# Kernel tuning notes

Hardware: AMD Instinct MI355X
Metric: run time of the kernel (lower is better)

## Reference

```python
import jax, jax.numpy as jnp
import numpy as np

EPS = 1e-5
TAU = 2.0
HEADS = 8
SCALE = 0.125


def _bn(y, g, b, m, v):
    # y: [TB, C, N]; per-channel eval-mode batchnorm
    inv = jax.lax.rsqrt(v + EPS)
    return (y - m[:, None]) * (g * inv)[:, None] + b[:, None]


def _lif(x_seq, vth):
    # spikingjelly MultiStepLIFNode: v += (x - v)/tau, spike = H(v - vth), hard reset v*(1-s)
    def step(mem, xt):
        mem = mem + (xt - mem) / TAU
        s = (mem >= vth).astype(xt.dtype)
        mem = mem * (1.0 - s)
        return mem, s
    _, spikes = jax.lax.scan(step, jnp.zeros_like(x_seq[0]), x_seq)
    return spikes


def setup_inputs() -> dict:
    key = jax.random.key(0)
    ks = jax.random.split(key, 8)
    T, B, C, H, W = 4, 16, 256, 32, 32
    d = {
        'x': jax.random.normal(ks[0], (T, B, C, H, W), jnp.float32),
        'res_attn': jnp.zeros((1,), jnp.float32),
    }
    for i, p in enumerate(['q', 'k', 'v']):
        d[p + '_w'] = jax.random.normal(ks[1 + i], (C, C), jnp.float32) * 0.02
        d[p + '_gamma'] = jnp.ones((C,), jnp.float32)
        d[p + '_beta'] = jnp.zeros((C,), jnp.float32)
        d[p + '_mean'] = jnp.zeros((C,), jnp.float32)
        d[p + '_var'] = jnp.ones((C,), jnp.float32)
    d['p_w'] = jax.random.normal(ks[4], (C, C), jnp.float32) * 0.02
    d['p_b'] = jnp.zeros((C,), jnp.float32)
    d['p_gamma'] = jnp.ones((C,), jnp.float32)
    d['p_beta'] = jnp.zeros((C,), jnp.float32)
    d['p_mean'] = jnp.zeros((C,), jnp.float32)
    d['p_var'] = jnp.ones((C,), jnp.float32)
    return d


def reference(x, res_attn, q_w, q_gamma, q_beta, q_mean, q_var,
              k_w, k_gamma, k_beta, k_mean, k_var,
              v_w, v_gamma, v_beta, v_mean, v_var,
              p_w, p_b, p_gamma, p_beta, p_mean, p_var):
    T, B, C, H, W = x.shape
    N = H * W
    d = C // HEADS
    x2 = x.reshape(T * B, C, N)

    def branch(w, g, b, m, v):
        y = _bn(jnp.einsum('oc,bcn->bon', w, x2), g, b, m, v).reshape(T, B, C, N)
        s = _lif(y, 1.0)  # [T,B,C,N]
        # -> [T,B,heads,N,d]
        return s.transpose(0, 1, 3, 2).reshape(T, B, N, HEADS, d).transpose(0, 1, 3, 2, 4)

    q = branch(q_w, q_gamma, q_beta, q_mean, q_var)
    k = branch(k_w, k_gamma, k_beta, k_mean, k_var)
    v = branch(v_w, v_gamma, v_beta, v_mean, v_var)

    kv = jnp.einsum('tbhnd,tbhne->tbhde', k, v)      # [T,B,h,d,d]
    attn = jnp.einsum('tbhnd,tbhde->tbhne', q, kv) * SCALE  # [T,B,h,N,d]
    xa = attn.transpose(0, 1, 2, 4, 3).reshape(T, B, C, N)
    xa = _lif(xa, 0.5)

    y = _bn(jnp.einsum('oc,bcn->bon', p_w, xa.reshape(T * B, C, N)) + p_b[:, None],
            p_gamma, p_beta, p_mean, p_var)
    out = _lif(y.reshape(T, B, C, H, W), 1.0)
    return (out, v)
```

## Files before the change

kernel.cpp:

```cpp
#include <hip/hip_runtime.h>
#include <stdint.h>

typedef unsigned int u32;
typedef unsigned short ushort_t;

#define T_ 4
#define B_ 16
#define C_ 256
#define N_ 1024
#define CN (C_ * N_)
#define M_ELEMS (64 * C_ * N_)

#define OFF_S    0ull
#define OFF_XC   67108864ull
#define OFF_SC   67108864ull
#define OFF_KV   134217728ull
#define OFF_BNS  136314880ull
#define OFF_WC   136331264ull
#define OFF_WPC  137510912ull

typedef __attribute__((ext_vector_type(8))) short bf16x8;
typedef __attribute__((ext_vector_type(4))) float f32x4;

#define SWZ(c) (((c) & ~3) | (((c) & 3) ^ (((c) >> 2) & 3) ^ (((c) >> 4) & 3)))

__device__ __forceinline__ ushort_t f2bf(float f) {
  u32 u = __float_as_uint(f);
  u32 r = (u + 0x7FFFu + ((u >> 16) & 1u)) >> 16;
  return (ushort_t)r;
}
__device__ __forceinline__ float bf2f(ushort_t h) { return __uint_as_float((u32)h << 16); }

__device__ __forceinline__ void async_copy16(const void* g, void* l) {
  __builtin_amdgcn_global_load_lds(
      (const __attribute__((address_space(1))) u32*)g,
      (__attribute__((address_space(3))) u32*)l, 16, 0, 0);
}

__device__ __forceinline__ void mfma_grp(const ushort_t* Ap, int aoff,
                                         bf16x8 b0, bf16x8 b1, bf16x8 b2, bf16x8 b3,
                                         f32x4* acc) {
  bf16x8 a0 = *(const bf16x8*)&Ap[aoff + 0 * 16 * 32];
  bf16x8 a1 = *(const bf16x8*)&Ap[aoff + 1 * 16 * 32];
  bf16x8 a2 = *(const bf16x8*)&Ap[aoff + 2 * 16 * 32];
  bf16x8 a3 = *(const bf16x8*)&Ap[aoff + 3 * 16 * 32];
  acc[0]  = __builtin_amdgcn_mfma_f32_16x16x32_bf16(a0, b0, acc[0],  0, 0, 0);
  acc[1]  = __builtin_amdgcn_mfma_f32_16x16x32_bf16(a0, b1, acc[1],  0, 0, 0);
  acc[2]  = __builtin_amdgcn_mfma_f32_16x16x32_bf16(a0, b2, acc[2],  0, 0, 0);
  acc[3]  = __builtin_amdgcn_mfma_f32_16x16x32_bf16(a0, b3, acc[3],  0, 0, 0);
  acc[4]  = __builtin_amdgcn_mfma_f32_16x16x32_bf16(a1, b0, acc[4],  0, 0, 0);
  acc[5]  = __builtin_amdgcn_mfma_f32_16x16x32_bf16(a1, b1, acc[5],  0, 0, 0);
  acc[6]  = __builtin_amdgcn_mfma_f32_16x16x32_bf16(a1, b2, acc[6],  0, 0, 0);
  acc[7]  = __builtin_amdgcn_mfma_f32_16x16x32_bf16(a1, b3, acc[7],  0, 0, 0);
  acc[8]  = __builtin_amdgcn_mfma_f32_16x16x32_bf16(a2, b0, acc[8],  0, 0, 0);
  acc[9]  = __builtin_amdgcn_mfma_f32_16x16x32_bf16(a2, b1, acc[9],  0, 0, 0);
  acc[10] = __builtin_amdgcn_mfma_f32_16x16x32_bf16(a2, b2, acc[10], 0, 0, 0);
  acc[11] = __builtin_amdgcn_mfma_f32_16x16x32_bf16(a2, b3, acc[11], 0, 0, 0);
  acc[12] = __builtin_amdgcn_mfma_f32_16x16x32_bf16(a3, b0, acc[12], 0, 0, 0);
  acc[13] = __builtin_amdgcn_mfma_f32_16x16x32_bf16(a3, b1, acc[13], 0, 0, 0);
  acc[14] = __builtin_amdgcn_mfma_f32_16x16x32_bf16(a3, b2, acc[14], 0, 0, 0);
  acc[15] = __builtin_amdgcn_mfma_f32_16x16x32_bf16(a3, b3, acc[15], 0, 0, 0);
}

__global__ void bn_prep(const float* __restrict__ qg, const float* __restrict__ qb2, const float* __restrict__ qm, const float* __restrict__ qv,
                        const float* __restrict__ kg, const float* __restrict__ kb, const float* __restrict__ km, const float* __restrict__ kvv,
                        const float* __restrict__ vg, const float* __restrict__ vb, const float* __restrict__ vm, const float* __restrict__ vv,
                        const float* __restrict__ pbias,
                        const float* __restrict__ pg, const float* __restrict__ pbt, const float* __restrict__ pm, const float* __restrict__ pv,
                        float* __restrict__ bns) {
  int i = threadIdx.x;
  int br = i >> 8, c = i & 255;
  const float *g, *bt, *m, *v;
  float bias = 0.f;
  if (br == 0)      { g = qg; bt = qb2; m = qm; v = qv; }
  else if (br == 1) { g = kg; bt = kb;  m = km; v = kvv; }
  else if (br == 2) { g = vg; bt = vb;  m = vm; v = vv; }
  else              { g = pg; bt = pbt; m = pm; v = pv; bias = pbias[c]; }
  float sc = g[c] / sqrtf(v[c] + 1e-5f);
  float sh = bt[c] + (bias - m[c]) * sc;
  float rcp = (sc != 0.f) ? (1.f / sc) : 0.f;
  *(float4*)&bns[4 * i] = make_float4(sc, sh, rcp, 0.f);
}

__global__ __launch_bounds__(256) void convert_w(const float* __restrict__ qw, const float* __restrict__ kw,
                                                 const float* __restrict__ vw, const float* __restrict__ pw,
                                                 ushort_t* __restrict__ Wc, ushort_t* __restrict__ Wpc) {
  int id = blockIdx.x * 256 + threadIdx.x;
  int br = id >> 16, o = (id >> 8) & 255, c = id & 255;
  const float* w = (br == 0) ? qw : (br == 1) ? kw : (br == 2) ? vw : pw;
  float f = w[o * 256 + c];
  ushort_t hi = f2bf(f);
  ushort_t lo = f2bf(f - bf2f(hi));
  if (br < 3) {
    ushort_t* d = Wc + (size_t)br * 196608 + (size_t)o * 768 + c;
    d[0] = hi; d[256] = lo; d[512] = hi;
  } else {
    ushort_t* d = Wpc + (size_t)o * 512 + c;
    d[0] = hi; d[256] = lo;
  }
}

__global__ __launch_bounds__(256) void convert_x(const float* __restrict__ x, ushort_t* __restrict__ Xc) {
  __shared__ ushort_t hi[32][260];
  __shared__ ushort_t lo[32][260];
  int bid = blockIdx.x;
  int nc = bid & 3, kb = (bid >> 2) & 7, tb = bid >> 5;
  int t = threadIdx.x;
  int n0 = nc * 256;
  const float* xb = x + (size_t)tb * CN + (size_t)(kb * 32) * N_ + n0;
#pragma unroll
  for (int p = 0; p < 8; ++p) {
    int k = p * 4 + (t >> 6);
    int n4 = (t & 63) * 4;
    float4 v = *(const float4*)&xb[(size_t)k * N_ + n4];
    ushort_t h0 = f2bf(v.x), h1 = f2bf(v.y), h2 = f2bf(v.z), h3 = f2bf(v.w);
    short4 hv = make_short4((short)h0, (short)h1, (short)h2, (short)h3);
    short4 lv = make_short4((short)f2bf(v.x - bf2f(h0)), (short)f2bf(v.y - bf2f(h1)),
                            (short)f2bf(v.z - bf2f(h2)), (short)f2bf(v.w - bf2f(h3)));
    *(short4*)&hi[k][n4] = hv;
    *(short4*)&lo[k][n4] = lv;
  }
  __syncthreads();
  ushort_t* Hs = Xc + ((size_t)(tb * 16 + kb) * 1024 + n0) * 32;
  ushort_t* Ls = Xc + ((size_t)(tb * 16 + 8 + kb) * 1024 + n0) * 32;
  int kq = t & 3;
#pragma unroll
  for (int q = 0; q < 4; ++q) {
    int n = q * 64 + (t >> 2);
    u32 a0 = (u32)hi[kq * 8 + 0][n] | ((u32)hi[kq * 8 + 1][n] << 16);
    u32 a1 = (u32)hi[kq * 8 + 2][n] | ((u32)hi[kq * 8 + 3][n] << 16);
    u32 a2 = (u32)hi[kq * 8 + 4][n] | ((u32)hi[kq * 8 + 5][n] << 16);
    u32 a3 = (u32)hi[kq * 8 + 6][n] | ((u32)hi[kq * 8 + 7][n] << 16);
    *(uint4*)(Hs + (size_t)n * 32 + kq * 8) = make_uint4(a0, a1, a2, a3);
    u32 b0 = (u32)lo[kq * 8 + 0][n] | ((u32)lo[kq * 8 + 1][n] << 16);
    u32 b1 = (u32)lo[kq * 8 + 2][n] | ((u32)lo[kq * 8 + 3][n] << 16);
    u32 b2 = (u32)lo[kq * 8 + 4][n] | ((u32)lo[kq * 8 + 5][n] << 16);
    u32 b3 = (u32)lo[kq * 8 + 6][n] | ((u32)lo[kq * 8 + 7][n] << 16);
    *(uint4*)(Ls + (size_t)n * 32 + kq * 8) = make_uint4(b0, b1, b2, b3);
  }
}

__global__ __launch_bounds__(256, 3) void gemm_qkv_lif(
    const ushort_t* __restrict__ Wc, const ushort_t* __restrict__ Xc,
    const float* __restrict__ bns, uint8_t* __restrict__ S) {
  __shared__ ushort_t Ah[2][4096];
  __shared__ ushort_t Xl[2][4096];
  __shared__ ushort_t Bh[2][4096];
  const int nt = blockIdx.x, mt = blockIdx.y, b = blockIdx.z;
  const int br = mt >> 1, rh = mt & 1;
  const ushort_t* Ab = Wc + (size_t)br * 196608 + (size_t)(rh * 128) * 768;
  const int tid = threadIdx.x;
  const int lane = tid & 63;
  const int quad = lane >> 4, r = lane & 15;
  const int w = tid >> 6;
  const int moff = (w & 1) * 64, noff = (w >> 1) * 64;
  const int c0 = tid, c1 = tid + 256;
  const int s0 = SWZ(c0), s1 = SWZ(c1);
  const int qx = quad ^ (r & 3) ^ ((r >> 2) & 3);
  const int aoff = (moff + r) * 32 + qx * 8;
  const int boff = (noff + r) * 32 + qx * 8;

  f32x4 acc[16];
#pragma unroll
  for (int f = 0; f < 16; ++f) acc[f] = (f32x4){0.f, 0.f, 0.f, 0.f};

  for (int t = 0; t < 4; ++t) {
    const ushort_t* Xtb = Xc + (size_t)(t * 16 + b) * 16 * 32768 + (size_t)(nt * 128) * 32;
    for (int p = 0; p < 4; ++p) {
      const ushort_t* AcH = Ab + p * 64;
      const ushort_t* AcL = Ab + 256 + p * 64;
      const ushort_t* Bh0 = Xtb + (size_t)(2 * p) * 32768;
      const ushort_t* Bh1 = Bh0 + 32768;
      async_copy16(AcH + (size_t)(c0 >> 2) * 768 + (s0 & 3) * 8,      &Ah[0][c0 * 8]);
      async_copy16(AcH + (size_t)(c1 >> 2) * 768 + (s1 & 3) * 8,      &Ah[0][c1 * 8]);
      async_copy16(AcH + (size_t)(c0 >> 2) * 768 + 32 + (s0 & 3) * 8, &Ah[1][c0 * 8]);
      async_copy16(AcH + (size_t)(c1 >> 2) * 768 + 32 + (s1 & 3) * 8, &Ah[1][c1 * 8]);
      async_copy16(AcL + (size_t)(c0 >> 2) * 768 + (s0 & 3) * 8,      &Xl[0][c0 * 8]);
      async_copy16(AcL + (size_t)(c1 >> 2) * 768 + (s1 & 3) * 8,      &Xl[0][c1 * 8]);
      async_copy16(AcL + (size_t)(c0 >> 2) * 768 + 32 + (s0 & 3) * 8, &Xl[1][c0 * 8]);
      async_copy16(AcL + (size_t)(c1 >> 2) * 768 + 32 + (s1 & 3) * 8, &Xl[1][c1 * 8]);
      async_copy16(Bh0 + s0 * 8, &Bh[0][c0 * 8]);
      async_copy16(Bh0 + s1 * 8, &Bh[0][c1 * 8]);
      async_copy16(Bh1 + s0 * 8, &Bh[1][c0 * 8]);
      async_copy16(Bh1 + s1 * 8, &Bh[1][c1 * 8]);
      __syncthreads();
      {
        bf16x8 b0 = *(const bf16x8*)&Bh[0][boff + 0 * 16 * 32];
        bf16x8 b1 = *(const bf16x8*)&Bh[0][boff + 1 * 16 * 32];
        bf16x8 b2 = *(const bf16x8*)&Bh[0][boff + 2 * 16 * 32];
        bf16x8 b3 = *(const bf16x8*)&Bh[0][boff + 3 * 16 * 32];
        mfma_grp(&Ah[0][0], aoff, b0, b1, b2, b3, acc);
        mfma_grp(&Xl[0][0], aoff, b0, b1, b2, b3, acc);
      }
      {
        bf16x8 b0 = *(const bf16x8*)&Bh[1][boff + 0 * 16 * 32];
        bf16x8 b1 = *(const bf16x8*)&Bh[1][boff + 1 * 16 * 32];
        bf16x8 b2 = *(const bf16x8*)&Bh[1][boff + 2 * 16 * 32];
        bf16x8 b3 = *(const bf16x8*)&Bh[1][boff + 3 * 16 * 32];
        mfma_grp(&Ah[1][0], aoff, b0, b1, b2, b3, acc);
        mfma_grp(&Xl[1][0], aoff, b0, b1, b2, b3, acc);
      }
      __syncthreads();
      const ushort_t* Bl0 = Xtb + (size_t)(8 + 2 * p) * 32768;
      const ushort_t* Bl1 = Bl0 + 32768;
      async_copy16(Bl0 + s0 * 8, &Xl[0][c0 * 8]);
      async_copy16(Bl0 + s1 * 8, &Xl[0][c1 * 8]);
      async_copy16(Bl1 + s0 * 8, &Xl[1][c0 * 8]);
      async_copy16(Bl1 + s1 * 8, &Xl[1][c1 * 8]);
      __syncthreads();
      {
        bf16x8 b0 = *(const bf16x8*)&Xl[0][boff + 0 * 16 * 32];
        bf16x8 b1 = *(const bf16x8*)&Xl[0][boff + 1 * 16 * 32];
        bf16x8 b2 = *(const bf16x8*)&Xl[0][boff + 2 * 16 * 32];
        bf16x8 b3 = *(const bf16x8*)&Xl[0][boff + 3 * 16 * 32];
        mfma_grp(&Ah[0][0], aoff, b0, b1, b2, b3, acc);
      }
      {
        bf16x8 b0 = *(const bf16x8*)&Xl[1][boff + 0 * 16 * 32];
        bf16x8 b1 = *(const bf16x8*)&Xl[1][boff + 1 * 16 * 32];
        bf16x8 b2 = *(const bf16x8*)&Xl[1][boff + 2 * 16 * 32];
        bf16x8 b3 = *(const bf16x8*)&Xl[1][boff + 3 * 16 * 32];
        mfma_grp(&Ah[1][0], aoff, b0, b1, b2, b3, acc);
      }
      __syncthreads();
    }
    uint8_t* Sb = S + (size_t)br * M_ELEMS + (size_t)(t * 16 + b) * CN;
#pragma unroll
    for (int i = 0; i < 4; ++i) {
#pragma unroll
      for (int rg = 0; rg < 4; ++rg) {
        int c = rh * 128 + moff + i * 16 + quad * 4 + rg;
        float4 bn = *(const float4*)&bns[4 * (br * 256 + c)];
        float hsc = 0.5f * bn.x;
        float hsh = 0.5f * bn.y;
        float rcp = bn.z;
        uint8_t* row = Sb + (size_t)c * N_ + nt * 128 + noff + r;
#pragma unroll
        for (int j = 0; j < 4; ++j) {
          float m = acc[i * 4 + j][rg] * hsc + hsh;
          uint8_t s = (m >= 1.0f) ? 1 : 0;
          row[j * 16] = s;
          acc[i * 4 + j][rg] = s ? 0.f : m * rcp;
        }
      }
    }
  }
}

__global__ __launch_bounds__(256) void transpose_v(const uint8_t* __restrict__ SV, float* __restrict__ vout) {
  size_t o4 = ((size_t)blockIdx.x * 256 + threadIdx.x) * 4;
  int dd = (int)(o4 & 31);
  int n = (int)((o4 >> 5) & 1023);
  int h = (int)((o4 >> 15) & 7);
  int tb = (int)(o4 >> 18);
  const uint8_t* src = SV + (size_t)tb * CN + (size_t)(h * 32 + dd) * N_ + n;
  *(float4*)(vout + o4) = make_float4((float)src[0], (float)src[(size_t)N_],
                                      (float)src[2 * (size_t)N_], (float)src[3 * (size_t)N_]);
}

__global__ __launch_bounds__(256) void kv_gram(const uint8_t* __restrict__ SK,
                                               const uint8_t* __restrict__ SV,
                                               float* __restrict__ KV) {
  __shared__ unsigned long long Kb[32][17];
  __shared__ unsigned long long Vb[32][17];
  const int tb = blockIdx.x >> 3, h = blockIdx.x & 7;
  const uint8_t* K = SK + (size_t)tb * CN + (size_t)h * 32 * N_;
  const uint8_t* V = SV + (size_t)tb * CN + (size_t)h * 32 * N_;
  const int tid = threadIdx.x;
  const int row = tid >> 3, c8 = tid & 7;
  uint8_t* Kb8 = (uint8_t*)&Kb[row][0];
  uint8_t* Vb8 = (uint8_t*)&Vb[row][0];
#pragma unroll
  for (int i = 0; i < 16; ++i) {
    int c = c8 + 8 * i;
    unsigned long long xk = *(const unsigned long long*)(K + (size_t)row * N_ + (size_t)c * 8);
    unsigned long long xv = *(const unsigned long long*)(V + (size_t)row * N_ + (size_t)c * 8);
    Kb8[c] = (uint8_t)((xk * 0x8040201008040201ull) >> 56);
    Vb8[c] = (uint8_t)((xv * 0x8040201008040201ull) >> 56);
  }
  __syncthreads();
  const int dd = tid >> 3, e0 = (tid & 7) * 4;
  int a0 = 0, a1 = 0, a2 = 0, a3 = 0;
#pragma unroll
  for (int c = 0; c < 16; ++c) {
    unsigned long long kd = Kb[dd][c];
    a0 += __popcll(kd & Vb[e0 + 0][c]);
    a1 += __popcll(kd & Vb[e0 + 1][c]);
    a2 += __popcll(kd & Vb[e0 + 2][c]);
    a3 += __popcll(kd & Vb[e0 + 3][c]);
  }
  float* o = KV + (size_t)(tb * 8 + h) * 1024 + dd * 32 + e0;
  o[0] = (float)a0; o[1] = (float)a1; o[2] = (float)a2; o[3] = (float)a3;
}

__global__ __launch_bounds__(256) void attn_lif(const uint8_t* __restrict__ SQ,
                                                const float* __restrict__ KV,
                                                ushort_t* __restrict__ Sc) {
  __shared__ float kvs[1024];
  const int bid = blockIdx.x;
  const int nb = bid & 15, h = (bid >> 4) & 7, b = bid >> 7;
  const int n0 = nb * 64;
  const int tid = threadIdx.x;
  const int nl = tid & 63, eg = tid >> 6;
  float mem[8];
#pragma unroll
  for (int j = 0; j < 8; ++j) mem[j] = 0.f;
  for (int t = 0; t < 4; ++t) {
    const float* kvp = KV + (size_t)((t * B_ + b) * 8 + h) * 1024;
    *(float4*)&kvs[tid * 4] = *(const float4*)&kvp[tid * 4];
    __syncthreads();
    const uint8_t* q = SQ + (size_t)(t * B_ + b) * CN + (size_t)h * 32 * N_ + n0 + nl;
    float val[8];
#pragma unroll
    for (int j = 0; j < 8; ++j) val[j] = 0.f;
#pragma unroll 4
    for (int dd = 0; dd < 32; ++dd) {
      float qv = (float)q[(size_t)dd * N_];
#pragma unroll
      for (int j = 0; j < 8; ++j) val[j] += qv * kvs[dd * 32 + eg * 8 + j];
    }
    ushort_t pk[8];
#pragma unroll
    for (int j = 0; j < 8; ++j) {
      float a = val[j] * 0.125f;
      mem[j] += (a - mem[j]) * 0.5f;
      int s = (mem[j] >= 0.5f);
      pk[j] = s ? (ushort_t)0x3F80 : (ushort_t)0;
      if (s) mem[j] = 0.f;
    }
    uint4 o;
    o.x = (u32)pk[0] | ((u32)pk[1] << 16);
    o.y = (u32)pk[2] | ((u32)pk[3] << 16);
    o.z = (u32)pk[4] | ((u32)pk[5] << 16);
    o.w = (u32)pk[6] | ((u32)pk[7] << 16);
    *(uint4*)(Sc + ((size_t)((t * B_ + b) * 8 + h) * 1024 + n0 + nl) * 32 + eg * 8) = o;
    __syncthreads();
  }
}

__global__ __launch_bounds__(256, 3) void gemm_p_lif(
    const ushort_t* __restrict__ Wpc, const ushort_t* __restrict__ Sc,
    const float* __restrict__ bns, float* __restrict__ out) {
  __shared__ ushort_t Ah[2][4096];
  __shared__ ushort_t Al[2][4096];
  __shared__ ushort_t Bs[2][4096];
  const int nt = blockIdx.x, mt = blockIdx.y, b = blockIdx.z;
  const ushort_t* Ab = Wpc + (size_t)(mt * 128) * 512;
  const int tid = threadIdx.x;
  const int lane = tid & 63;
  const int quad = lane >> 4, r = lane & 15;
  const int w = tid >> 6;
  const int moff = (w & 1) * 64, noff = (w >> 1) * 64;
  const int c0 = tid, c1 = tid + 256;
  const int s0 = SWZ(c0), s1 = SWZ(c1);
  const int qx = quad ^ (r & 3) ^ ((r >> 2) & 3);
  const int aoff = (moff + r) * 32 + qx * 8;
  const int boff = (noff + r) * 32 + qx * 8;
  f32x4 acc[16];
#pragma unroll
  for (int f = 0; f < 16; ++f) acc[f] = (f32x4){0.f, 0.f, 0.f, 0.f};

  for (int t = 0; t < 4; ++t) {
    const ushort_t* Stb = Sc + (size_t)(t * 16 + b) * 8 * 32768 + (size_t)(nt * 128) * 32;
    for (int p = 0; p < 4; ++p) {
      const ushort_t* AcH = Ab + p * 64;
      const ushort_t* AcL = Ab + 256 + p * 64;
      const ushort_t* Bb0 = Stb + (size_t)(2 * p) * 32768;
      const ushort_t* Bb1 = Bb0 + 32768;
      async_copy16(AcH + (size_t)(c0 >> 2) * 512 + (s0 & 3) * 8,      &Ah[0][c0 * 8]);
      async_copy16(AcH + (size_t)(c1 >> 2) * 512 + (s1 & 3) * 8,      &Ah[0][c1 * 8]);
      async_copy16(AcH + (size_t)(c0 >> 2) * 512 + 32 + (s0 & 3) * 8, &Ah[1][c0 * 8]);
      async_copy16(AcH + (size_t)(c1 >> 2) * 512 + 32 + (s1 & 3) * 8, &Ah[1][c1 * 8]);
      async_copy16(AcL + (size_t)(c0 >> 2) * 512 + (s0 & 3) * 8,      &Al[0][c0 * 8]);
      async_copy16(AcL + (size_t)(c1 >> 2) * 512 + (s1 & 3) * 8,      &Al[0][c1 * 8]);
      async_copy16(AcL + (size_t)(c0 >> 2) * 512 + 32 + (s0 & 3) * 8, &Al[1][c0 * 8]);
      async_copy16(AcL + (size_t)(c1 >> 2) * 512 + 32 + (s1 & 3) * 8, &Al[1][c1 * 8]);
      async_copy16(Bb0 + s0 * 8, &Bs[0][c0 * 8]);
      async_copy16(Bb0 + s1 * 8, &Bs[0][c1 * 8]);
      async_copy16(Bb1 + s0 * 8, &Bs[1][c0 * 8]);
      async_copy16(Bb1 + s1 * 8, &Bs[1][c1 * 8]);
      __syncthreads();
      {
        bf16x8 b0 = *(const bf16x8*)&Bs[0][boff + 0 * 16 * 32];
        bf16x8 b1 = *(const bf16x8*)&Bs[0][boff + 1 * 16 * 32];
        bf16x8 b2 = *(const bf16x8*)&Bs[0][boff + 2 * 16 * 32];
        bf16x8 b3 = *(const bf16x8*)&Bs[0][boff + 3 * 16 * 32];
        mfma_grp(&Ah[0][0], aoff, b0, b1, b2, b3, acc);
        mfma_grp(&Al[0][0], aoff, b0, b1, b2, b3, acc);
      }
      {
        bf16x8 b0 = *(const bf16x8*)&Bs[1][boff + 0 * 16 * 32];
        bf16x8 b1 = *(const bf16x8*)&Bs[1][boff + 1 * 16 * 32];
        bf16x8 b2 = *(const bf16x8*)&Bs[1][boff + 2 * 16 * 32];
        bf16x8 b3 = *(const bf16x8*)&Bs[1][boff + 3 * 16 * 32];
        mfma_grp(&Ah[1][0], aoff, b0, b1, b2, b3, acc);
        mfma_grp(&Al[1][0], aoff, b0, b1, b2, b3, acc);
      }
      __syncthreads();
    }
    float* Ob = out + (size_t)(t * 16 + b) * CN;
#pragma unroll
    for (int i = 0; i < 4; ++i) {
#pragma unroll
      for (int rg = 0; rg < 4; ++rg) {
        int c = mt * 128 + moff + i * 16 + quad * 4 + rg;
        float4 bn = *(const float4*)&bns[4 * (768 + c)];
        float hsc = 0.5f * bn.x;
        float hsh = 0.5f * bn.y;
        float rcp = bn.z;
        float* row2 = Ob + (size_t)c * N_ + nt * 128 + noff + r;
#pragma unroll
        for (int j = 0; j < 4; ++j) {
          float m = acc[i * 4 + j][rg] * hsc + hsh;
          int s = (m >= 1.0f);
          row2[j * 16] = s ? 1.0f : 0.0f;
          acc[i * 4 + j][rg] = s ? 0.f : m * rcp;
        }
      }
    }
  }
}

extern "C" void kernel_launch(void* const* d_in, const int* in_sizes, int n_in,
                              void* d_out, int out_size, void* d_ws, size_t ws_size,
                              hipStream_t stream) {
  const float* x   = (const float*)d_in[0];
  const float* qw  = (const float*)d_in[2];
  const float* qg  = (const float*)d_in[3];
  const float* qb  = (const float*)d_in[4];
  const float* qm  = (const float*)d_in[5];
  const float* qv  = (const float*)d_in[6];
  const float* kw  = (const float*)d_in[7];
  const float* kg  = (const float*)d_in[8];
  const float* kb  = (const float*)d_in[9];
  const float* km  = (const float*)d_in[10];
  const float* kvv = (const float*)d_in[11];
  const float* vw  = (const float*)d_in[12];
  const float* vg  = (const float*)d_in[13];
  const float* vb  = (const float*)d_in[14];
  const float* vm  = (const float*)d_in[15];
  const float* vv  = (const float*)d_in[16];
  const float* pw  = (const float*)d_in[17];
  const float* pb  = (const float*)d_in[18];
  const float* pg  = (const float*)d_in[19];
  const float* pbt = (const float*)d_in[20];
  const float* pm  = (const float*)d_in[21];
  const float* pv  = (const float*)d_in[22];

  float* out = (float*)d_out;
  float* vout = out + M_ELEMS;

  uint8_t* ws = (uint8_t*)d_ws;
  uint8_t* S   = ws + OFF_S;
  ushort_t* Xc = (ushort_t*)(ws + OFF_XC);
  ushort_t* Sc = (ushort_t*)(ws + OFF_SC);
  float* KV    = (float*)(ws + OFF_KV);
  float* BNS   = (float*)(ws + OFF_BNS);
  ushort_t* Wc  = (ushort_t*)(ws + OFF_WC);
  ushort_t* Wpc = (ushort_t*)(ws + OFF_WPC);

  bn_prep<<<dim3(1), dim3(1024), 0, stream>>>(qg, qb, qm, qv, kg, kb, km, kvv,
                                              vg, vb, vm, vv, pb, pg, pbt, pm, pv, BNS);
  convert_w<<<dim3(1024), dim3(256), 0, stream>>>(qw, kw, vw, pw, Wc, Wpc);
  convert_x<<<dim3(2048), dim3(256), 0, stream>>>(x, Xc);
  gemm_qkv_lif<<<dim3(8, 6, 16), dim3(256), 0, stream>>>(Wc, Xc, BNS, S);
  transpose_v<<<dim3(16384), dim3(256), 0, stream>>>(S + 2ull * M_ELEMS, vout);
  kv_gram<<<dim3(512), dim3(256), 0, stream>>>(S + 1ull * M_ELEMS, S + 2ull * M_ELEMS, KV);
  attn_lif<<<dim3(2048), dim3(256), 0, stream>>>(S, KV, Sc);
  gemm_p_lif<<<dim3(8, 2, 16), dim3(256), 0, stream>>>(Wpc, Sc, BNS, out);
}
```

Baseline: 404.9 us.

## Pipeline QKV and projection GEMM K-loops with a three-buffer async prefetch ring

Both LIF-fused GEMM kernels replace their load-everything-then-compute inner loops with a flat loop over K=32 stages. Each stage loads an A chunk and a B chunk into one of three LDS buffers, prefetching two stages ahead. Explicit vmcnt waits and raw s_barrier calls replace the per-phase __syncthreads, so global-to-LDS copies overlap the MFMA work. This trades coarser load batches and manual wait-count bookkeeping for less stall time. The bookkeeping is fragile if other memory ops, such as the epilogue stores, shift the outstanding counts.

```diff
diff --git a/kernel.cpp b/kernel.cpp
--- a/kernel.cpp
+++ b/kernel.cpp
@@ -23,6 +23,8 @@
 typedef __attribute__((ext_vector_type(4))) float f32x4;
 
 #define SWZ(c) (((c) & ~3) | (((c) & 3) ^ (((c) >> 2) & 3) ^ (((c) >> 4) & 3)))
+
+#define WAITV(N) asm volatile("s_waitcnt vmcnt(" #N ")" ::: "memory")
 
 __device__ __forceinline__ ushort_t f2bf(float f) {
   u32 u = __float_as_uint(f);
@@ -143,9 +145,7 @@
 __global__ __launch_bounds__(256, 3) void gemm_qkv_lif(
     const ushort_t* __restrict__ Wc, const ushort_t* __restrict__ Xc,
     const float* __restrict__ bns, uint8_t* __restrict__ S) {
-  __shared__ ushort_t Ah[2][4096];
-  __shared__ ushort_t Xl[2][4096];
-  __shared__ ushort_t Bh[2][4096];
+  __shared__ ushort_t L[3][8192];
   const int nt = blockIdx.x, mt = blockIdx.y, b = blockIdx.z;
   const int br = mt >> 1, rh = mt & 1;
   const ushort_t* Ab = Wc + (size_t)br * 196608 + (size_t)(rh * 128) * 768;
@@ -158,89 +158,70 @@
   const int s0 = SWZ(c0), s1 = SWZ(c1);
   const int qx = quad ^ (r & 3) ^ ((r >> 2) & 3);
   const int aoff = (moff + r) * 32 + qx * 8;
-  const int boff = (noff + r) * 32 + qx * 8;
+  const int boff = 4096 + (noff + r) * 32 + qx * 8;
+
+  auto STAGE = [&](int gS, int bi) {
+    const int tS = gS / 24;
+    const int jS = gS - tS * 24;
+    const ushort_t* Acol = Ab + jS * 32;
+    const int slab = (jS < 8) ? jS : (jS - 8);
+    const ushort_t* Bb = Xc + ((size_t)(tS * 16 + b) * 16 + slab) * 32768 +
+                         (size_t)(nt * 128) * 32;
+    ushort_t* Lb = &L[bi][0];
+    async_copy16(Acol + (size_t)(c0 >> 2) * 768 + (s0 & 3) * 8, Lb + c0 * 8);
+    async_copy16(Acol + (size_t)(c1 >> 2) * 768 + (s1 & 3) * 8, Lb + c1 * 8);
+    async_copy16(Bb + s0 * 8, Lb + 4096 + c0 * 8);
+    async_copy16(Bb + s1 * 8, Lb + 4096 + c1 * 8);
+  };
 
   f32x4 acc[16];
 #pragma unroll
   for (int f = 0; f < 16; ++f) acc[f] = (f32x4){0.f, 0.f, 0.f, 0.f};
 
-  for (int t = 0; t < 4; ++t) {
-    const ushort_t* Xtb = Xc + (size_t)(t * 16 + b) * 16 * 32768 + (size_t)(nt * 128) * 32;
-    for (int p = 0; p < 4; ++p) {
-      const ushort_t* AcH = Ab + p * 64;
-      const ushort_t* AcL = Ab + 256 + p * 64;
-      const ushort_t* Bh0 = Xtb + (size_t)(2 * p) * 32768;
-      const ushort_t* Bh1 = Bh0 + 32768;
-      async_copy16(AcH + (size_t)(c0 >> 2) * 768 + (s0 & 3) * 8,      &Ah[0][c0 * 8]);
-      async_copy16(AcH + (size_t)(c1 >> 2) * 768 + (s1 & 3) * 8,      &Ah[0][c1 * 8]);
-      async_copy16(AcH + (size_t)(c0 >> 2) * 768 + 32 + (s0 & 3) * 8, &Ah[1][c0 * 8]);
-      async_copy16(AcH + (size_t)(c1 >> 2) * 768 + 32 + (s1 & 3) * 8, &Ah[1][c1 * 8]);
-      async_copy16(AcL + (size_t)(c0 >> 2) * 768 + (s0 & 3) * 8,      &Xl[0][c0 * 8]);
-      async_copy16(AcL + (size_t)(c1 >> 2) * 768 + (s1 & 3) * 8,      &Xl[0][c1 * 8]);
-      async_copy16(AcL + (size_t)(c0 >> 2) * 768 + 32 + (s0 & 3) * 8, &Xl[1][c0 * 8]);
-      async_copy16(AcL + (size_t)(c1 >> 2) * 768 + 32 + (s1 & 3) * 8, &Xl[1][c1 * 8]);
-      async_copy16(Bh0 + s0 * 8, &Bh[0][c0 * 8]);
-      async_copy16(Bh0 + s1 * 8, &Bh[0][c1 * 8]);
-      async_copy16(Bh1 + s0 * 8, &Bh[1][c0 * 8]);
-      async_copy16(Bh1 + s1 * 8, &Bh[1][c1 * 8]);
-      __syncthreads();
-      {
-        bf16x8 b0 = *(const bf16x8*)&Bh[0][boff + 0 * 16 * 32];
-        bf16x8 b1 = *(const bf16x8*)&Bh[0][boff + 1 * 16 * 32];
-        bf16x8 b2 = *(const bf16x8*)&Bh[0][boff + 2 * 16 * 32];
-        bf16x8 b3 = *(const bf16x8*)&Bh[0][boff + 3 * 16 * 32];
-        mfma_grp(&Ah[0][0], aoff, b0, b1, b2, b3, acc);
-        mfma_grp(&Xl[0][0], aoff, b0, b1, b2, b3, acc);
-      }
-      {
-        bf16x8 b0 = *(const bf16x8*)&Bh[1][boff + 0 * 16 * 32];
-        bf16x8 b1 = *(const bf16x8*)&Bh[1][boff + 1 * 16 * 32];
-        bf16x8 b2 = *(const bf16x8*)&Bh[1][boff + 2 * 16 * 32];
-        bf16x8 b3 = *(const bf16x8*)&Bh[1][boff + 3 * 16 * 32];
-        mfma_grp(&Ah[1][0], aoff, b0, b1, b2, b3, acc);
-        mfma_grp(&Xl[1][0], aoff, b0, b1, b2, b3, acc);
-      }
-      __syncthreads();
-      const ushort_t* Bl0 = Xtb + (size_t)(8 + 2 * p) * 32768;
-      const ushort_t* Bl1 = Bl0 + 32768;
-      async_copy16(Bl0 + s0 * 8, &Xl[0][c0 * 8]);
-      async_copy16(Bl0 + s1 * 8, &Xl[0][c1 * 8]);
-      async_copy16(Bl1 + s0 * 8, &Xl[1][c0 * 8]);
-      async_copy16(Bl1 + s1 * 8, &Xl[1][c1 * 8]);
-      __syncthreads();
-      {
-        bf16x8 b0 = *(const bf16x8*)&Xl[0][boff + 0 * 16 * 32];
-        bf16x8 b1 = *(const bf16x8*)&Xl[0][boff + 1 * 16 * 32];
-        bf16x8 b2 = *(const bf16x8*)&Xl[0][boff + 2 * 16 * 32];
-        bf16x8 b3 = *(const bf16x8*)&Xl[0][boff + 3 * 16 * 32];
-        mfma_grp(&Ah[0][0], aoff, b0, b1, b2, b3, acc);
-      }
-      {
-        bf16x8 b0 = *(const bf16x8*)&Xl[1][boff + 0 * 16 * 32];
-        bf16x8 b1 = *(const bf16x8*)&Xl[1][boff + 1 * 16 * 32];
-        bf16x8 b2 = *(const bf16x8*)&Xl[1][boff + 2 * 16 * 32];
-        bf16x8 b3 = *(const bf16x8*)&Xl[1][boff + 3 * 16 * 32];
-        mfma_grp(&Ah[1][0], aoff, b0, b1, b2, b3, acc);
-      }
-      __syncthreads();
-    }
-    uint8_t* Sb = S + (size_t)br * M_ELEMS + (size_t)(t * 16 + b) * CN;
-#pragma unroll
-    for (int i = 0; i < 4; ++i) {
-#pragma unroll
-      for (int rg = 0; rg < 4; ++rg) {
-        int c = rh * 128 + moff + i * 16 + quad * 4 + rg;
-        float4 bn = *(const float4*)&bns[4 * (br * 256 + c)];
-        float hsc = 0.5f * bn.x;
-        float hsh = 0.5f * bn.y;
-        float rcp = bn.z;
-        uint8_t* row = Sb + (size_t)c * N_ + nt * 128 + noff + r;
-#pragma unroll
-        for (int j = 0; j < 4; ++j) {
-          float m = acc[i * 4 + j][rg] * hsc + hsh;
-          uint8_t s = (m >= 1.0f) ? 1 : 0;
-          row[j * 16] = s;
-          acc[i * 4 + j][rg] = s ? 0.f : m * rcp;
+  STAGE(0, 0);
+  STAGE(1, 1);
+  int cb = 0, sb = 2;
+
+#pragma unroll 1
+  for (int g = 0; g < 96; ++g) {
+    __builtin_amdgcn_s_barrier();
+    __builtin_amdgcn_sched_barrier(0);
+    if (g < 94) STAGE(g + 2, sb);
+    if (g < 94)      { WAITV(8); }
+    else if (g == 94){ WAITV(4); }
+    else             { WAITV(0); }
+    __builtin_amdgcn_s_barrier();
+    __builtin_amdgcn_sched_barrier(0);
+    {
+      const ushort_t* Lc = &L[cb][0];
+      bf16x8 q0 = *(const bf16x8*)&Lc[boff + 0 * 512];
+      bf16x8 q1 = *(const bf16x8*)&Lc[boff + 1 * 512];
+      bf16x8 q2 = *(const bf16x8*)&Lc[boff + 2 * 512];
+      bf16x8 q3 = *(const bf16x8*)&Lc[boff + 3 * 512];
+      mfma_grp(Lc, aoff, q0, q1, q2, q3, acc);
+    }
+    cb = (cb == 2) ? 0 : cb + 1;
+    sb = (sb == 2) ? 0 : sb + 1;
+    const int t = g / 24;
+    if (g - t * 24 == 23) {
+      uint8_t* Sb = S + (size_t)br * M_ELEMS + (size_t)(t * 16 + b) * CN;
+#pragma unroll
+      for (int i = 0; i < 4; ++i) {
+#pragma unroll
+        for (int rg = 0; rg < 4; ++rg) {
+          int c = rh * 128 + moff + i * 16 + quad * 4 + rg;
+          float4 bn = *(const float4*)&bns[4 * (br * 256 + c)];
+          float hsc = 0.5f * bn.x;
+          float hsh = 0.5f * bn.y;
+          float rcp = bn.z;
+          uint8_t* row = Sb + (size_t)c * N_ + nt * 128 + noff + r;
+#pragma unroll
+          for (int j = 0; j < 4; ++j) {
+            float m = acc[i * 4 + j][rg] * hsc + hsh;
+            uint8_t s = (m >= 1.0f) ? 1 : 0;
+            row[j * 16] = s;
+            acc[i * 4 + j][rg] = s ? 0.f : m * rcp;
+          }
         }
       }
     }
@@ -341,9 +322,7 @@
 __global__ __launch_bounds__(256, 3) void gemm_p_lif(
     const ushort_t* __restrict__ Wpc, const ushort_t* __restrict__ Sc,
     const float* __restrict__ bns, float* __restrict__ out) {
-  __shared__ ushort_t Ah[2][4096];
-  __shared__ ushort_t Al[2][4096];
-  __shared__ ushort_t Bs[2][4096];
+  __shared__ ushort_t L[3][8192];
   const int nt = blockIdx.x, mt = blockIdx.y, b = blockIdx.z;
   const ushort_t* Ab = Wpc + (size_t)(mt * 128) * 512;
   const int tid = threadIdx.x;
@@ -355,66 +334,70 @@
   const int s0 = SWZ(c0), s1 = SWZ(c1);
   const int qx = quad ^ (r & 3) ^ ((r >> 2) & 3);
   const int aoff = (moff + r) * 32 + qx * 8;
-  const int boff = (noff + r) * 32 + qx * 8;
+  const int boff = 4096 + (noff + r) * 32 + qx * 8;
+
+  auto STAGE = [&](int gS, int bi) {
+    const int tS = gS >> 4;
+    const int jS = gS & 15;
+    const ushort_t* Acol = Ab + jS * 32;
+    const int slab = jS & 7;
+    const ushort_t* Bb = Sc + ((size_t)(tS * 16 + b) * 8 + slab) * 32768 +
+                         (size_t)(nt * 128) * 32;
+    ushort_t* Lb = &L[bi][0];
+    async_copy16(Acol + (size_t)(c0 >> 2) * 512 + (s0 & 3) * 8, Lb + c0 * 8);
+    async_copy16(Acol + (size_t)(c1 >> 2) * 512 + (s1 & 3) * 8, Lb + c1 * 8);
+    async_copy16(Bb + s0 * 8, Lb + 4096 + c0 * 8);
+    async_copy16(Bb + s1 * 8, Lb + 4096 + c1 * 8);
+  };
+
   f32x4 acc[16];
 #pragma unroll
   for (int f = 0; f < 16; ++f) acc[f] = (f32x4){0.f, 0.f, 0.f, 0.f};
 
-  for (int t = 0; t < 4; ++t) {
-    const ushort_t* Stb = Sc + (size_t)(t * 16 + b) * 8 * 32768 + (size_t)(nt * 128) * 32;
-    for (int p = 0; p < 4; ++p) {
-      const ushort_t* AcH = Ab + p * 64;
-      const ushort_t* AcL = Ab + 256 + p * 64;
-      const ushort_t* Bb0 = Stb + (size_t)(2 * p) * 32768;
-      const ushort_t* Bb1 = Bb0 + 32768;
-      async_copy16(AcH + (size_t)(c0 >> 2) * 512 + (s0 & 3) * 8,      &Ah[0][c0 * 8]);
-      async_copy16(AcH + (size_t)(c1 >> 2) * 512 + (s1 & 3) * 8,      &Ah[0][c1 * 8]);
-      async_copy16(AcH + (size_t)(c0 >> 2) * 512 + 32 + (s0 & 3) * 8, &Ah[1][c0 * 8]);
-      async_copy16(AcH + (size_t)(c1 >> 2) * 512 + 32 + (s1 & 3) * 8, &Ah[1][c1 * 8]);
-      async_copy16(AcL + (size_t)(c0 >> 2) * 512 + (s0 & 3) * 8,      &Al[0][c0 * 8]);
-      async_copy16(AcL + (size_t)(c1 >> 2) * 512 + (s1 & 3) * 8,      &Al[0][c1 * 8]);
-      async_copy16(AcL + (size_t)(c0 >> 2) * 512 + 32 + (s0 & 3) * 8, &Al[1][c0 * 8]);
-      async_copy16(AcL + (size_t)(c1 >> 2) * 512 + 32 + (s1 & 3) * 8, &Al[1][c1 * 8]);
-      async_copy16(Bb0 + s0 * 8, &Bs[0][c0 * 8]);
-      async_copy16(Bb0 + s1 * 8, &Bs[0][c1 * 8]);
-      async_copy16(Bb1 + s0 * 8, &Bs[1][c0 * 8]);
-      async_copy16(Bb1 + s1 * 8, &Bs[1][c1 * 8]);
-      __syncthreads();
-      {
-        bf16x8 b0 = *(const bf16x8*)&Bs[0][boff + 0 * 16 * 32];
-        bf16x8 b1 = *(const bf16x8*)&Bs[0][boff + 1 * 16 * 32];
-        bf16x8 b2 = *(const bf16x8*)&Bs[0][boff + 2 * 16 * 32];
-        bf16x8 b3 = *(const bf16x8*)&Bs[0][boff + 3 * 16 * 32];
-        mfma_grp(&Ah[0][0], aoff, b0, b1, b2, b3, acc);
-        mfma_grp(&Al[0][0], aoff, b0, b1, b2, b3, acc);
-      }
-      {
-        bf16x8 b0 = *(const bf16x8*)&Bs[1][boff + 0 * 16 * 32];
-        bf16x8 b1 = *(const bf16x8*)&Bs[1][boff + 1 * 16 * 32];
-        bf16x8 b2 = *(const bf16x8*)&Bs[1][boff + 2 * 16 * 32];
-        bf16x8 b3 = *(const bf16x8*)&Bs[1][boff + 3 * 16 * 32];
-        mfma_grp(&Ah[1][0], aoff, b0, b1, b2, b3, acc);
-        mfma_grp(&Al[1][0], aoff, b0, b1, b2, b3, acc);
-      }
-      __syncthreads();
-    }
-    float* Ob = out + (size_t)(t * 16 + b) * CN;
-#pragma unroll
-    for (int i = 0; i < 4; ++i) {
-#pragma unroll
-      for (int rg = 0; rg < 4; ++rg) {
-        int c = mt * 128 + moff + i * 16 + quad * 4 + rg;
-        float4 bn = *(const float4*)&bns[4 * (768 + c)];
-        float hsc = 0.5f * bn.x;
-        float hsh = 0.5f * bn.y;
-        float rcp = bn.z;
-        float* row2 = Ob + (size_t)c * N_ + nt * 128 + noff + r;
-#pragma unroll
-        for (int j = 0; j < 4; ++j) {
-          float m = acc[i * 4 + j][rg] * hsc + hsh;
-          int s = (m >= 1.0f);
-          row2[j * 16] = s ? 1.0f : 0.0f;
-          acc[i * 4 + j][rg] = s ? 0.f : m * rcp;
+  STAGE(0, 0);
+  STAGE(1, 1);
+  int cb = 0, sb = 2;
+
+#pragma unroll 1
+  for (int g = 0; g < 64; ++g) {
+    __builtin_amdgcn_s_barrier();
+    __builtin_amdgcn_sched_barrier(0);
+    if (g < 62) STAGE(g + 2, sb);
+    if (g < 62)      { WAITV(8); }
+    else if (g == 62){ WAITV(4); }
+    else             { WAITV(0); }
+    __builtin_amdgcn_s_barrier();
+    __builtin_amdgcn_sched_barrier(0);
+    {
+      const ushort_t* Lc = &L[cb][0];
+      bf16x8 q0 = *(const bf16x8*)&Lc[boff + 0 * 512];
+      bf16x8 q1 = *(const bf16x8*)&Lc[boff + 1 * 512];
+      bf16x8 q2 = *(const bf16x8*)&Lc[boff + 2 * 512];
+      bf16x8 q3 = *(const bf16x8*)&Lc[boff + 3 * 512];
+      mfma_grp(Lc, aoff, q0, q1, q2, q3, acc);
+    }
+    cb = (cb == 2) ? 0 : cb + 1;
+    sb = (sb == 2) ? 0 : sb + 1;
+    if ((g & 15) == 15) {
+      const int t = g >> 4;
+      float* Ob = out + (size_t)(t * 16 + b) * CN;
+#pragma unroll
+      for (int i = 0; i < 4; ++i) {
+#pragma unroll
+        for (int rg = 0; rg < 4; ++rg) {
+          int c = mt * 128 + moff + i * 16 + quad * 4 + rg;
+          float4 bn = *(const float4*)&bns[4 * (768 + c)];
+          float hsc = 0.5f * bn.x;
+          float hsh = 0.5f * bn.y;
+          float rcp = bn.z;
+          float* row2 = Ob + (size_t)c * N_ + nt * 128 + noff + r;
+#pragma unroll
+          for (int j = 0; j < 4; ++j) {
+            float m = acc[i * 4 + j][rg] * hsc + hsh;
+            int s = (m >= 1.0f);
+            row2[j * 16] = s ? 1.0f : 0.0f;
+            acc[i * 4 + j][rg] = s ? 0.f : m * rcp;
+          }
         }
       }
     }
```

Measured after the change: 418.1 us. 3.3% more time.
